# Optimization experiments

Hardware: AMD Instinct MI355X
Metric: run time of the kernel (lower is better)

## Reference

```python
import jax, jax.numpy as jnp
import numpy as np

N_NODES = 50000
N_EDGES = 800000
NUM_GRAPHS = 1024
IN_DIM = 25
DIM = 64
STEPS = 3


def setup_inputs() -> dict:
    key = jax.random.key(0)
    ks = jax.random.split(key, 16)
    s = 0.1
    return {
        "x": jax.random.normal(ks[0], (N_NODES, IN_DIM), dtype=jnp.float32),
        "edge_index": jax.random.randint(ks[1], (2, N_EDGES), 0, N_NODES),
        "batch": jnp.sort(jax.random.randint(ks[2], (N_NODES,), 0, NUM_GRAPHS)),
        "W0": jax.random.normal(ks[3], (IN_DIM, DIM), dtype=jnp.float32) * s,
        "b0": jnp.zeros((DIM,), jnp.float32),
        "Wc": jax.random.normal(ks[4], (DIM, DIM), dtype=jnp.float32) * s,
        "bc": jnp.zeros((DIM,), jnp.float32),
        "Wih": jax.random.normal(ks[5], (4 * DIM, 2 * DIM), dtype=jnp.float32) * s,
        "Whh": jax.random.normal(ks[6], (4 * DIM, DIM), dtype=jnp.float32) * s,
        "bih": jnp.zeros((4 * DIM,), jnp.float32),
        "bhh": jnp.zeros((4 * DIM,), jnp.float32),
        "W1": jax.random.normal(ks[7], (2 * DIM, DIM), dtype=jnp.float32) * s,
        "b1": jnp.zeros((DIM,), jnp.float32),
        "W2": jax.random.normal(ks[8], (DIM, 1), dtype=jnp.float32) * s,
        "b2": jnp.zeros((1,), jnp.float32),
    }


def _lstm_cell(xin, h, c, Wih, Whh, bih, bhh):
    gates = xin @ Wih.T + h @ Whh.T + bih + bhh  # [B, 4*DIM]
    i, f, g, o = jnp.split(gates, 4, axis=-1)
    i, f, o = jax.nn.sigmoid(i), jax.nn.sigmoid(f), jax.nn.sigmoid(o)
    g = jnp.tanh(g)
    c = f * c + i * g
    h = o * jnp.tanh(c)
    return h, c


def reference(x, edge_index, batch, W0, b0, Wc, bc, Wih, Whh, bih, bhh, W1, b1, W2, b2):
    n = x.shape[0]
    # lin0 + relu
    h = jax.nn.relu(x @ W0 + b0)
    # GCNConv: x @ W, add self loops, symmetric normalization, scatter-add
    hw = h @ Wc
    loops = jnp.arange(n, dtype=edge_index.dtype)
    row = jnp.concatenate([edge_index[0], loops])  # sources
    col = jnp.concatenate([edge_index[1], loops])  # targets
    deg = jax.ops.segment_sum(jnp.ones_like(row, dtype=hw.dtype), col, num_segments=n)
    dinv = jnp.where(deg > 0, jax.lax.rsqrt(deg), 0.0)
    norm = dinv[row] * dinv[col]
    msg = hw[row] * norm[:, None]  # [E+N, DIM] gather
    agg = jax.ops.segment_sum(msg, col, num_segments=n) + bc
    h = jax.nn.relu(agg)
    # Set2Set pooling with LSTM, 3 processing steps
    B = NUM_GRAPHS
    q_star = jnp.zeros((B, 2 * DIM), h.dtype)
    hs = jnp.zeros((B, DIM), h.dtype)
    cs = jnp.zeros((B, DIM), h.dtype)
    for _ in range(STEPS):
        hs, cs = _lstm_cell(q_star, hs, cs, Wih, Whh, bih, bhh)
        q = hs  # [B, DIM]
        e = jnp.sum(h * q[batch], axis=-1)  # [N]
        emax = jax.ops.segment_max(e, batch, num_segments=B)
        a = jnp.exp(e - emax[batch])
        asum = jax.ops.segment_sum(a, batch, num_segments=B)
        a = a / asum[batch]
        r = jax.ops.segment_sum(a[:, None] * h, batch, num_segments=B)  # [B, DIM]
        q_star = jnp.concatenate([q, r], axis=-1)
    out = jax.nn.relu(q_star @ W1 + b1)
    out = out @ W2 + b2
    return out.reshape(-1)
```

## Files before the change

### kernel.cpp

```cpp
#include <hip/hip_runtime.h>
#include <hip/hip_fp16.h>
#include <math.h>

#define N_NODES 50000
#define N_EDGES 800000
#define NGRAPH  1024
#define IN_DIM  25
#define DIM     64

#define NBKB 782
#define CAP  1536
#define NBIN 391
#define CROWS 128

__device__ inline float wsum(float v) {
#pragma unroll
  for (int off = 32; off > 0; off >>= 1) v += __shfl_xor(v, off, 64);
  return v;
}
__device__ inline float sigmoidf(float x) { return 1.f / (1.f + expf(-x)); }

__global__ __launch_bounds__(512) void k_bin(const int* __restrict__ ei,
    int* __restrict__ gcur, int* __restrict__ pairs,
    const float* __restrict__ Wih, const float* __restrict__ Whh,
    float* __restrict__ WT) {
  __shared__ int hist[NBKB];
  __shared__ int sbase[NBKB];
  __shared__ int lbase[NBKB];
  __shared__ int sorted[2048];
  int t = threadIdx.x;
  if (blockIdx.x == NBIN) {
    for (int i = t; i < 3 * DIM * 4 * DIM; i += 512) {
      int k = i >> 8, tt = i & 255;
      WT[i] = (k < 2 * DIM) ? Wih[tt * 2 * DIM + k] : Whh[tt * DIM + (k - 2 * DIM)];
    }
    return;
  }
  int base = blockIdx.x * 2048;
  for (int i = t; i < NBKB; i += 512) hist[i] = 0;
  __syncthreads();
  int n = min(2048, N_EDGES - base);
  const int4* r4 = (const int4*)(ei + base);
  const int4* c4 = (const int4*)(ei + N_EDGES + base);
  int pk[4], bkt[4], rank[4];
  {
    bool ok = t * 4 < n;
    int4 rv, cv;
    if (ok) { rv = r4[t]; cv = c4[t]; }
#pragma unroll
    for (int u = 0; u < 4; u++) {
      if (ok) {
        int row = (&rv.x)[u], col = (&cv.x)[u];
        int b = col >> 6;
        bkt[u] = b;
        rank[u] = atomicAdd(&hist[b], 1);
        pk[u] = (int)(((unsigned)b << 22) | ((unsigned)(col & 63) << 16) | (unsigned)row);
      } else {
        bkt[u] = -1;
      }
    }
  }
  __syncthreads();
  if (t < 64) {
    int v[13];
    int loc = 0;
#pragma unroll
    for (int i = 0; i < 13; i++) {
      int idx = t * 13 + i;
      v[i] = (idx < NBKB) ? hist[idx] : 0;
      loc += v[i];
    }
    int x = loc;
#pragma unroll
    for (int d = 1; d < 64; d <<= 1) {
      int y = __shfl_up(x, d, 64);
      if (t >= d) x += y;
    }
    int excl = x - loc;
#pragma unroll
    for (int i = 0; i < 13; i++) {
      int idx = t * 13 + i;
      if (idx < NBKB) sbase[idx] = excl;
      excl += v[i];
    }
  }
  __syncthreads();
#pragma unroll
  for (int u = 0; u < 4; u++)
    if (bkt[u] >= 0) sorted[sbase[bkt[u]] + rank[u]] = pk[u];
  for (int i = t; i < NBKB; i += 512)
    lbase[i] = hist[i] ? atomicAdd(&gcur[i], hist[i]) : 0;
  __syncthreads();
  for (int i = t; i < n; i += 512) {
    int p = sorted[i];
    int b = ((unsigned)p) >> 22;
    int gpos = lbase[b] + (i - sbase[b]);
    if (gpos < CAP) pairs[(size_t)b * CAP + gpos] = p & 0x3FFFFF;
  }
}

__global__ __launch_bounds__(256) void k_lin0(const float* __restrict__ x,
    const float* __restrict__ W0, const float* __restrict__ b0,
    const float* __restrict__ Wc, const int* __restrict__ pairs,
    const int* __restrict__ gcur, float* __restrict__ dinv,
    __half* __restrict__ hw16) {
  __shared__ float sx[64][IN_DIM + 1];
  __shared__ float sW0[IN_DIM][DIM];
  __shared__ float sh[64][DIM + 4];
  __shared__ float sWc[DIM][DIM];
  __shared__ int histd[64];
  int t = threadIdx.x;
  int row0 = blockIdx.x * 64;
  if (t < 64) histd[t] = 0;
  __syncthreads();
  for (int i = t; i < 64 * IN_DIM; i += 256) {
    int r = i / IN_DIM, k = i - r * IN_DIM;
    int row = row0 + r;
    sx[r][k] = (row < N_NODES) ? x[row * IN_DIM + k] : 0.f;
  }
  for (int i = t; i < IN_DIM * DIM; i += 256) sW0[i >> 6][i & 63] = W0[i];
  for (int i = t; i < DIM * DIM; i += 256) sWc[i >> 6][i & 63] = Wc[i];
  {
    int ne = min(gcur[blockIdx.x], CAP);
    const int* pp = pairs + (size_t)blockIdx.x * CAP;
    const int4* pp4 = (const int4*)pp;
    int ne4 = ne >> 2;
    for (int i = t; i < ne4; i += 256) {
      int4 p4 = pp4[i];
      atomicAdd(&histd[(p4.x >> 16) & 63], 1);
      atomicAdd(&histd[(p4.y >> 16) & 63], 1);
      atomicAdd(&histd[(p4.z >> 16) & 63], 1);
      atomicAdd(&histd[(p4.w >> 16) & 63], 1);
    }
    for (int i = (ne4 << 2) + t; i < ne; i += 256)
      atomicAdd(&histd[(pp[i] >> 16) & 63], 1);
  }
  __syncthreads();
  int tc = (t & 15) * 4;
  int tr = (t >> 4) * 4;
  float acc[4][4];
  {
    float4 bb = *(const float4*)&b0[tc];
#pragma unroll
    for (int i = 0; i < 4; i++) {
      acc[i][0] = bb.x; acc[i][1] = bb.y; acc[i][2] = bb.z; acc[i][3] = bb.w;
    }
  }
#pragma unroll
  for (int k = 0; k < IN_DIM; k++) {
    float4 w = *(const float4*)&sW0[k][tc];
#pragma unroll
    for (int i = 0; i < 4; i++) {
      float a = sx[tr + i][k];
      acc[i][0] += a * w.x; acc[i][1] += a * w.y;
      acc[i][2] += a * w.z; acc[i][3] += a * w.w;
    }
  }
#pragma unroll
  for (int i = 0; i < 4; i++) {
    sh[tr + i][tc + 0] = fmaxf(acc[i][0], 0.f);
    sh[tr + i][tc + 1] = fmaxf(acc[i][1], 0.f);
    sh[tr + i][tc + 2] = fmaxf(acc[i][2], 0.f);
    sh[tr + i][tc + 3] = fmaxf(acc[i][3], 0.f);
  }
  __syncthreads();
#pragma unroll
  for (int i = 0; i < 4; i++) acc[i][0] = acc[i][1] = acc[i][2] = acc[i][3] = 0.f;
#pragma unroll 8
  for (int k = 0; k < DIM; k++) {
    float4 w = *(const float4*)&sWc[k][tc];
#pragma unroll
    for (int i = 0; i < 4; i++) {
      float a = sh[tr + i][k];
      acc[i][0] += a * w.x; acc[i][1] += a * w.y;
      acc[i][2] += a * w.z; acc[i][3] += a * w.w;
    }
  }
  if (t < 64) {
    int node = row0 + t;
    if (node < N_NODES) dinv[node] = rsqrtf((float)(histd[t] + 1));
  }
  float2* hwf2 = (float2*)hw16;
#pragma unroll
  for (int i = 0; i < 4; i++) {
    int row = row0 + tr + i;
    if (row < N_NODES) {
      float dv = rsqrtf((float)(histd[tr + i] + 1));
      float2 st;
      ((__half2*)&st)[0] = __floats2half2_rn(acc[i][0] * dv, acc[i][1] * dv);
      ((__half2*)&st)[1] = __floats2half2_rn(acc[i][2] * dv, acc[i][3] * dv);
      hwf2[(size_t)row * 16 + (t & 15)] = st;
    }
  }
}

__global__ __launch_bounds__(256) void k_agg(const int* __restrict__ pairs,
    const int* __restrict__ gcur, const __half* __restrict__ hw16,
    const float* __restrict__ dinv, const float4* __restrict__ bc4,
    __half* __restrict__ h16) {
  __shared__ unsigned short rows[CAP];
  __shared__ int hist[64];
  __shared__ int off[65];
  __shared__ int cur[64];
  int b = blockIdx.x, t = threadIdx.x;
  int lane = t & 63, wave = t >> 6, q = lane >> 4, ql = lane & 15;
  int qid = (wave << 2) + q;
  if (t < 64) hist[t] = 0;
  __syncthreads();
  int ne = min(gcur[b], CAP);
  const int* pp = pairs + (size_t)b * CAP;
  const int4* pp4 = (const int4*)pp;
  int ne4 = ne >> 2;
  for (int i = t; i < ne4; i += 256) {
    int4 p4 = pp4[i];
    atomicAdd(&hist[(p4.x >> 16) & 63], 1);
    atomicAdd(&hist[(p4.y >> 16) & 63], 1);
    atomicAdd(&hist[(p4.z >> 16) & 63], 1);
    atomicAdd(&hist[(p4.w >> 16) & 63], 1);
  }
  for (int i = (ne4 << 2) + t; i < ne; i += 256)
    atomicAdd(&hist[(pp[i] >> 16) & 63], 1);
  __syncthreads();
  if (t < 64) {
    int v = hist[t];
    int x = v;
#pragma unroll
    for (int d = 1; d < 64; d <<= 1) {
      int y = __shfl_up(x, d, 64);
      if (t >= d) x += y;
    }
    off[t] = x - v;
    cur[t] = x - v;
    if (t == 63) off[64] = x;
  }
  __syncthreads();
  for (int i = t; i < ne4; i += 256) {
    int4 p4 = pp4[i];
#pragma unroll
    for (int u = 0; u < 4; u++) {
      int p = (&p4.x)[u];
      int slot = atomicAdd(&cur[(p >> 16) & 63], 1);
      rows[slot] = (unsigned short)(p & 0xFFFF);
    }
  }
  for (int i = (ne4 << 2) + t; i < ne; i += 256) {
    int p = pp[i];
    int slot = atomicAdd(&cur[(p >> 16) & 63], 1);
    rows[slot] = (unsigned short)(p & 0xFFFF);
  }
  __syncthreads();
  const float2* hwf2 = (const float2*)hw16;
  float4 bb = bc4[ql];
  for (int nl = qid; nl < 64; nl += 16) {
    int node = b * 64 + nl;
    if (node >= N_NODES) continue;
    int s0 = off[nl], e0 = off[nl + 1];
    float4 a0, a1, a2, a3;
    {
      float2 raw = hwf2[(size_t)node * 16 + ql];
      float2 f0 = __half22float2(((const __half2*)&raw)[0]);
      float2 f1 = __half22float2(((const __half2*)&raw)[1]);
      a0 = make_float4(f0.x, f0.y, f1.x, f1.y);
      a1 = make_float4(0.f, 0.f, 0.f, 0.f); a2 = a1; a3 = a1;
    }
    int j = s0;
    for (; j + 4 <= e0; j += 4) {
      int r0 = rows[j], r1 = rows[j + 1], r2 = rows[j + 2], r3 = rows[j + 3];
      float2 w0 = hwf2[(size_t)r0 * 16 + ql];
      float2 w1 = hwf2[(size_t)r1 * 16 + ql];
      float2 w2 = hwf2[(size_t)r2 * 16 + ql];
      float2 w3 = hwf2[(size_t)r3 * 16 + ql];
      float2 f;
      f = __half22float2(((const __half2*)&w0)[0]); a0.x += f.x; a0.y += f.y;
      f = __half22float2(((const __half2*)&w0)[1]); a0.z += f.x; a0.w += f.y;
      f = __half22float2(((const __half2*)&w1)[0]); a1.x += f.x; a1.y += f.y;
      f = __half22float2(((const __half2*)&w1)[1]); a1.z += f.x; a1.w += f.y;
      f = __half22float2(((const __half2*)&w2)[0]); a2.x += f.x; a2.y += f.y;
      f = __half22float2(((const __half2*)&w2)[1]); a2.z += f.x; a2.w += f.y;
      f = __half22float2(((const __half2*)&w3)[0]); a3.x += f.x; a3.y += f.y;
      f = __half22float2(((const __half2*)&w3)[1]); a3.z += f.x; a3.w += f.y;
    }
    for (; j < e0; j++) {
      int r = rows[j];
      float2 w = hwf2[(size_t)r * 16 + ql];
      float2 f;
      f = __half22float2(((const __half2*)&w)[0]); a0.x += f.x; a0.y += f.y;
      f = __half22float2(((const __half2*)&w)[1]); a0.z += f.x; a0.w += f.y;
    }
    float di = dinv[node];
    float ox = fmaxf(((a0.x + a1.x) + (a2.x + a3.x)) * di + bb.x, 0.f);
    float oy = fmaxf(((a0.y + a1.y) + (a2.y + a3.y)) * di + bb.y, 0.f);
    float oz = fmaxf(((a0.z + a1.z) + (a2.z + a3.z)) * di + bb.z, 0.f);
    float ow = fmaxf(((a0.w + a1.w) + (a2.w + a3.w)) * di + bb.w, 0.f);
    float2 st;
    ((__half2*)&st)[0] = __floats2half2_rn(ox, oy);
    ((__half2*)&st)[1] = __floats2half2_rn(oz, ow);
    ((float2*)h16)[(size_t)node * 16 + ql] = st;
  }
}

__global__ __launch_bounds__(256) void k_set2set(
    const __half* __restrict__ h16, const int* __restrict__ batch,
    const float* __restrict__ WT, const float* __restrict__ bih,
    const float* __restrict__ bhh, const float* __restrict__ W1,
    const float* __restrict__ b1, const float* __restrict__ W2,
    const float* __restrict__ b2, float* __restrict__ out) {
  int b = blockIdx.x, t = threadIdx.x;
  int wave = t >> 6, lane = t & 63;
  int q = lane >> 4, ql = lane & 15;
  int qid = (wave << 2) + q;
  __shared__ float2 hcf2[CROWS * 16];
  __shared__ float qs[2 * DIM];
  __shared__ float hsl[DIM], csl[DIM];
  __shared__ float gates[4 * DIM];
  __shared__ float red[16 * DIM];
  __shared__ float lred[16], wmax[16];
  __shared__ int seg[2];
  const float2* h2 = (const float2*)h16;
  if (t < 2) {
    int g = b + t;
    int lo = 0, hi = N_NODES;
    if (g == NGRAPH) lo = N_NODES;
    else while (lo < hi) { int mid = (lo + hi) >> 1; if (batch[mid] < g) lo = mid + 1; else hi = mid; }
    seg[t] = lo;
  }
  if (t < 2 * DIM) qs[t] = 0.f;
  if (t < DIM) { hsl[t] = 0.f; csl[t] = 0.f; }
  __syncthreads();
  int s = seg[0], eend = seg[1];
  int nc = min(eend - s, CROWS);
  for (int i = t; i < nc * 16; i += 256)
    hcf2[i] = h2[(size_t)(s + (i >> 4)) * 16 + (i & 15)];
  __syncthreads();
  float bsum = bih[t] + bhh[t];
  for (int step = 0; step < 3; step++) {
    float g = bsum;
    if (step > 0) {
      const float* wp = WT + t;
      float g1 = 0.f;
#pragma unroll 8
      for (int k = 0; k < 2 * DIM; k += 2) {
        g += qs[k] * wp[k * 4 * DIM];
        g1 += qs[k + 1] * wp[(k + 1) * 4 * DIM];
      }
#pragma unroll 8
      for (int k = 0; k < DIM; k += 2) {
        g += hsl[k] * wp[(2 * DIM + k) * 4 * DIM];
        g1 += hsl[k + 1] * wp[(2 * DIM + k + 1) * 4 * DIM];
      }
      g += g1;
    }
    gates[t] = g;
    __syncthreads();
    if (t < DIM) {
      float ig = sigmoidf(gates[t]);
      float fg = sigmoidf(gates[DIM + t]);
      float gg = tanhf(gates[2 * DIM + t]);
      float og = sigmoidf(gates[3 * DIM + t]);
      float c = fg * csl[t] + ig * gg;
      csl[t] = c;
      float hh = og * tanhf(c);
      hsl[t] = hh;
      qs[t] = hh;
    }
    __syncthreads();
    float4 qf = *(const float4*)&hsl[4 * ql];
    float m_w = -INFINITY, l_w = 0.f;
    float4 racc = make_float4(0.f, 0.f, 0.f, 0.f);
    for (int j = s + qid; j < eend; j += 16) {
      int lj = j - s;
      float2 raw = (lj < CROWS) ? hcf2[lj * 16 + ql]
                                : h2[(size_t)j * 16 + ql];
      float2 f0 = __half22float2(((const __half2*)&raw)[0]);
      float2 f1 = __half22float2(((const __half2*)&raw)[1]);
      float p = f0.x * qf.x + f0.y * qf.y + f1.x * qf.z + f1.y * qf.w;
#pragma unroll
      for (int off = 1; off < 16; off <<= 1) p += __shfl_xor(p, off, 64);
      float m_new = fmaxf(m_w, p);
      float scale = __expf(m_w - m_new);
      float a = __expf(p - m_new);
      racc.x = racc.x * scale + a * f0.x;
      racc.y = racc.y * scale + a * f0.y;
      racc.z = racc.z * scale + a * f1.x;
      racc.w = racc.w * scale + a * f1.y;
      l_w = l_w * scale + a;
      m_w = m_new;
    }
    *(float4*)&red[qid * DIM + 4 * ql] = racc;
    if (ql == 0) { lred[qid] = l_w; wmax[qid] = m_w; }
    __syncthreads();
    if (t < DIM) {
      float m_b = -1e30f;
      for (int i = 0; i < 16; i++) m_b = fmaxf(m_b, wmax[i]);
      float r = 0.f, l = 0.f;
      for (int i = 0; i < 16; i++) {
        float e = __expf(wmax[i] - m_b);
        r += red[i * DIM + t] * e;
        l += lred[i] * e;
      }
      qs[DIM + t] = (l > 0.f) ? r / l : 0.f;
    }
    __syncthreads();
  }
  if (t < DIM) {
    float acc = b1[t];
#pragma unroll
    for (int k = 0; k < 2 * DIM; k++) acc += qs[k] * W1[k * DIM + t];
    acc = fmaxf(acc, 0.f);
    float v = wsum(acc * W2[t]);
    if (t == 0) out[b] = v + b2[0];
  }
}

extern "C" void kernel_launch(void* const* d_in, const int* in_sizes, int n_in,
                              void* d_out, int out_size, void* d_ws, size_t ws_size,
                              hipStream_t stream) {
  const float* x    = (const float*)d_in[0];
  const int*   ei   = (const int*)d_in[1];
  const int*   batch= (const int*)d_in[2];
  const float* W0   = (const float*)d_in[3];
  const float* b0   = (const float*)d_in[4];
  const float* Wc   = (const float*)d_in[5];
  const float* bc   = (const float*)d_in[6];
  const float* Wih  = (const float*)d_in[7];
  const float* Whh  = (const float*)d_in[8];
  const float* bih  = (const float*)d_in[9];
  const float* bhh  = (const float*)d_in[10];
  const float* W1   = (const float*)d_in[11];
  const float* b1   = (const float*)d_in[12];
  const float* W2   = (const float*)d_in[13];
  const float* b2   = (const float*)d_in[14];
  float* out = (float*)d_out;

  __half* hw16 = (__half*)d_ws;
  __half* h16  = hw16 + (size_t)N_NODES * DIM;
  float* dinv  = (float*)(h16 + (size_t)N_NODES * DIM);
  float* WT    = dinv + N_NODES;
  int* gcur    = (int*)(WT + 3 * DIM * 4 * DIM);
  int* pairs   = gcur + NBKB + 2;

  hipMemsetAsync(gcur, 0, NBKB * sizeof(int), stream);
  k_bin<<<NBIN + 1, 512, 0, stream>>>(ei, gcur, pairs, Wih, Whh, WT);
  k_lin0<<<NBKB, 256, 0, stream>>>(x, W0, b0, Wc, pairs, gcur, dinv, hw16);
  k_agg<<<NBKB, 256, 0, stream>>>(pairs, gcur, hw16, dinv, (const float4*)bc, h16);
  k_set2set<<<NGRAPH, 256, 0, stream>>>(h16, batch, WT, bih, bhh, W1, b1, W2, b2, out);
}
```

Measured before the change: 191.9 us.

## Batch four graphs per set2set block, enlarge binning blocks, unroll gather by eight

The set2set kernel now handles four graphs per block. Each LSTM weight load is reused across four gate accumulators, and each graph's attention pass is split across four quarter-wave groups, cutting redundant weight traffic and the block count. The binning kernel processes 4096 edges per 1024-thread block, which halves the number of blocks and global atomics. The aggregation gather loop gets an eight-way unrolled path for more loads in flight. The trade-offs are less parallelism per graph in the attention loop and only 256 set2set blocks to fill the device.

```diff
diff --git a/kernel.cpp b/kernel.cpp
--- a/kernel.cpp
+++ b/kernel.cpp
@@ -10,8 +10,10 @@
 
 #define NBKB 782
 #define CAP  1536
-#define NBIN 391
-#define CROWS 128
+#define EPB  4096
+#define NBIN 196
+#define GPB  4
+#define CROW1 64
 
 __device__ inline float wsum(float v) {
 #pragma unroll
@@ -20,26 +22,26 @@
 }
 __device__ inline float sigmoidf(float x) { return 1.f / (1.f + expf(-x)); }
 
-__global__ __launch_bounds__(512) void k_bin(const int* __restrict__ ei,
+__global__ __launch_bounds__(1024) void k_bin(const int* __restrict__ ei,
     int* __restrict__ gcur, int* __restrict__ pairs,
     const float* __restrict__ Wih, const float* __restrict__ Whh,
     float* __restrict__ WT) {
   __shared__ int hist[NBKB];
   __shared__ int sbase[NBKB];
   __shared__ int lbase[NBKB];
-  __shared__ int sorted[2048];
+  __shared__ int sorted[EPB];
   int t = threadIdx.x;
   if (blockIdx.x == NBIN) {
-    for (int i = t; i < 3 * DIM * 4 * DIM; i += 512) {
+    for (int i = t; i < 3 * DIM * 4 * DIM; i += 1024) {
       int k = i >> 8, tt = i & 255;
       WT[i] = (k < 2 * DIM) ? Wih[tt * 2 * DIM + k] : Whh[tt * DIM + (k - 2 * DIM)];
     }
     return;
   }
-  int base = blockIdx.x * 2048;
-  for (int i = t; i < NBKB; i += 512) hist[i] = 0;
-  __syncthreads();
-  int n = min(2048, N_EDGES - base);
+  int base = blockIdx.x * EPB;
+  for (int i = t; i < NBKB; i += 1024) hist[i] = 0;
+  __syncthreads();
+  int n = min(EPB, N_EDGES - base);
   const int4* r4 = (const int4*)(ei + base);
   const int4* c4 = (const int4*)(ei + N_EDGES + base);
   int pk[4], bkt[4], rank[4];
@@ -88,10 +90,10 @@
 #pragma unroll
   for (int u = 0; u < 4; u++)
     if (bkt[u] >= 0) sorted[sbase[bkt[u]] + rank[u]] = pk[u];
-  for (int i = t; i < NBKB; i += 512)
+  for (int i = t; i < NBKB; i += 1024)
     lbase[i] = hist[i] ? atomicAdd(&gcur[i], hist[i]) : 0;
   __syncthreads();
-  for (int i = t; i < n; i += 512) {
+  for (int i = t; i < n; i += 1024) {
     int p = sorted[i];
     int b = ((unsigned)p) >> 22;
     int gpos = lbase[b] + (i - sbase[b]);
@@ -264,6 +266,35 @@
       a1 = make_float4(0.f, 0.f, 0.f, 0.f); a2 = a1; a3 = a1;
     }
     int j = s0;
+    for (; j + 8 <= e0; j += 8) {
+      int r0 = rows[j], r1 = rows[j + 1], r2 = rows[j + 2], r3 = rows[j + 3];
+      int r4_ = rows[j + 4], r5 = rows[j + 5], r6 = rows[j + 6], r7 = rows[j + 7];
+      float2 w0 = hwf2[(size_t)r0 * 16 + ql];
+      float2 w1 = hwf2[(size_t)r1 * 16 + ql];
+      float2 w2 = hwf2[(size_t)r2 * 16 + ql];
+      float2 w3 = hwf2[(size_t)r3 * 16 + ql];
+      float2 w4 = hwf2[(size_t)r4_ * 16 + ql];
+      float2 w5 = hwf2[(size_t)r5 * 16 + ql];
+      float2 w6 = hwf2[(size_t)r6 * 16 + ql];
+      float2 w7 = hwf2[(size_t)r7 * 16 + ql];
+      float2 f;
+      f = __half22float2(((const __half2*)&w0)[0]); a0.x += f.x; a0.y += f.y;
+      f = __half22float2(((const __half2*)&w0)[1]); a0.z += f.x; a0.w += f.y;
+      f = __half22float2(((const __half2*)&w1)[0]); a1.x += f.x; a1.y += f.y;
+      f = __half22float2(((const __half2*)&w1)[1]); a1.z += f.x; a1.w += f.y;
+      f = __half22float2(((const __half2*)&w2)[0]); a2.x += f.x; a2.y += f.y;
+      f = __half22float2(((const __half2*)&w2)[1]); a2.z += f.x; a2.w += f.y;
+      f = __half22float2(((const __half2*)&w3)[0]); a3.x += f.x; a3.y += f.y;
+      f = __half22float2(((const __half2*)&w3)[1]); a3.z += f.x; a3.w += f.y;
+      f = __half22float2(((const __half2*)&w4)[0]); a0.x += f.x; a0.y += f.y;
+      f = __half22float2(((const __half2*)&w4)[1]); a0.z += f.x; a0.w += f.y;
+      f = __half22float2(((const __half2*)&w5)[0]); a1.x += f.x; a1.y += f.y;
+      f = __half22float2(((const __half2*)&w5)[1]); a1.z += f.x; a1.w += f.y;
+      f = __half22float2(((const __half2*)&w6)[0]); a2.x += f.x; a2.y += f.y;
+      f = __half22float2(((const __half2*)&w6)[1]); a2.z += f.x; a2.w += f.y;
+      f = __half22float2(((const __half2*)&w7)[0]); a3.x += f.x; a3.y += f.y;
+      f = __half22float2(((const __half2*)&w7)[1]); a3.z += f.x; a3.w += f.y;
+    }
     for (; j + 4 <= e0; j += 4) {
       int r0 = rows[j], r1 = rows[j + 1], r2 = rows[j + 2], r3 = rows[j + 3];
       float2 w0 = hwf2[(size_t)r0 * 16 + ql];
@@ -309,67 +340,81 @@
   int wave = t >> 6, lane = t & 63;
   int q = lane >> 4, ql = lane & 15;
   int qid = (wave << 2) + q;
-  __shared__ float2 hcf2[CROWS * 16];
-  __shared__ float qs[2 * DIM];
-  __shared__ float hsl[DIM], csl[DIM];
-  __shared__ float gates[4 * DIM];
+  __shared__ float2 hcf2[GPB * CROW1 * 16];
+  __shared__ float qs4[GPB * 2 * DIM];
+  __shared__ float hsl4[GPB * DIM], csl4[GPB * DIM];
+  __shared__ float gates4[GPB * 4 * DIM];
   __shared__ float red[16 * DIM];
   __shared__ float lred[16], wmax[16];
-  __shared__ int seg[2];
+  __shared__ int seg[GPB + 1];
   const float2* h2 = (const float2*)h16;
-  if (t < 2) {
-    int g = b + t;
+  if (t < GPB + 1) {
+    int g = b * GPB + t;
     int lo = 0, hi = N_NODES;
-    if (g == NGRAPH) lo = N_NODES;
+    if (g >= NGRAPH) lo = N_NODES;
     else while (lo < hi) { int mid = (lo + hi) >> 1; if (batch[mid] < g) lo = mid + 1; else hi = mid; }
     seg[t] = lo;
   }
-  if (t < 2 * DIM) qs[t] = 0.f;
-  if (t < DIM) { hsl[t] = 0.f; csl[t] = 0.f; }
-  __syncthreads();
-  int s = seg[0], eend = seg[1];
-  int nc = min(eend - s, CROWS);
-  for (int i = t; i < nc * 16; i += 256)
-    hcf2[i] = h2[(size_t)(s + (i >> 4)) * 16 + (i & 15)];
+  for (int i = t; i < GPB * 2 * DIM; i += 256) qs4[i] = 0.f;
+  if (t < GPB * DIM) { hsl4[t] = 0.f; csl4[t] = 0.f; }
+  __syncthreads();
+  for (int i = t; i < GPB * CROW1 * 16; i += 256) {
+    int g = i >> 10;
+    int lj = (i >> 4) & (CROW1 - 1);
+    int row = seg[g] + lj;
+    if (row < seg[g + 1]) hcf2[i] = h2[(size_t)row * 16 + (i & 15)];
+  }
   __syncthreads();
   float bsum = bih[t] + bhh[t];
+  int ga = qid & 3;
+  int sub = qid >> 2;
   for (int step = 0; step < 3; step++) {
-    float g = bsum;
+    float g0 = bsum, g1 = bsum, g2 = bsum, g3 = bsum;
     if (step > 0) {
       const float* wp = WT + t;
-      float g1 = 0.f;
-#pragma unroll 8
-      for (int k = 0; k < 2 * DIM; k += 2) {
-        g += qs[k] * wp[k * 4 * DIM];
-        g1 += qs[k + 1] * wp[(k + 1) * 4 * DIM];
+#pragma unroll 4
+      for (int k = 0; k < 2 * DIM; k++) {
+        float w = wp[k * 4 * DIM];
+        g0 += qs4[0 * 2 * DIM + k] * w;
+        g1 += qs4[1 * 2 * DIM + k] * w;
+        g2 += qs4[2 * 2 * DIM + k] * w;
+        g3 += qs4[3 * 2 * DIM + k] * w;
       }
-#pragma unroll 8
-      for (int k = 0; k < DIM; k += 2) {
-        g += hsl[k] * wp[(2 * DIM + k) * 4 * DIM];
-        g1 += hsl[k + 1] * wp[(2 * DIM + k + 1) * 4 * DIM];
+#pragma unroll 4
+      for (int k = 0; k < DIM; k++) {
+        float w = wp[(2 * DIM + k) * 4 * DIM];
+        g0 += hsl4[0 * DIM + k] * w;
+        g1 += hsl4[1 * DIM + k] * w;
+        g2 += hsl4[2 * DIM + k] * w;
+        g3 += hsl4[3 * DIM + k] * w;
       }
-      g += g1;
-    }
-    gates[t] = g;
+    }
+    gates4[0 * 4 * DIM + t] = g0;
+    gates4[1 * 4 * DIM + t] = g1;
+    gates4[2 * 4 * DIM + t] = g2;
+    gates4[3 * 4 * DIM + t] = g3;
     __syncthreads();
-    if (t < DIM) {
-      float ig = sigmoidf(gates[t]);
-      float fg = sigmoidf(gates[DIM + t]);
-      float gg = tanhf(gates[2 * DIM + t]);
-      float og = sigmoidf(gates[3 * DIM + t]);
-      float c = fg * csl[t] + ig * gg;
-      csl[t] = c;
+    {
+      int g = wave, j = lane;
+      const float* gg_ = &gates4[g * 4 * DIM];
+      float ig = sigmoidf(gg_[j]);
+      float fg = sigmoidf(gg_[DIM + j]);
+      float gv = tanhf(gg_[2 * DIM + j]);
+      float og = sigmoidf(gg_[3 * DIM + j]);
+      float c = fg * csl4[g * DIM + j] + ig * gv;
+      csl4[g * DIM + j] = c;
       float hh = og * tanhf(c);
-      hsl[t] = hh;
-      qs[t] = hh;
+      hsl4[g * DIM + j] = hh;
+      qs4[g * 2 * DIM + j] = hh;
     }
     __syncthreads();
-    float4 qf = *(const float4*)&hsl[4 * ql];
+    float4 qf = *(const float4*)&hsl4[ga * DIM + 4 * ql];
     float m_w = -INFINITY, l_w = 0.f;
     float4 racc = make_float4(0.f, 0.f, 0.f, 0.f);
-    for (int j = s + qid; j < eend; j += 16) {
-      int lj = j - s;
-      float2 raw = (lj < CROWS) ? hcf2[lj * 16 + ql]
+    int s_g = seg[ga], e_g = seg[ga + 1];
+    for (int j = s_g + sub; j < e_g; j += 4) {
+      int lj = j - s_g;
+      float2 raw = (lj < CROW1) ? hcf2[(ga * CROW1 + lj) * 16 + ql]
                                 : h2[(size_t)j * 16 + ql];
       float2 f0 = __half22float2(((const __half2*)&raw)[0]);
       float2 f1 = __half22float2(((const __half2*)&raw)[1]);
@@ -389,26 +434,31 @@
     *(float4*)&red[qid * DIM + 4 * ql] = racc;
     if (ql == 0) { lred[qid] = l_w; wmax[qid] = m_w; }
     __syncthreads();
-    if (t < DIM) {
+    {
+      int g = wave, j = lane;
       float m_b = -1e30f;
-      for (int i = 0; i < 16; i++) m_b = fmaxf(m_b, wmax[i]);
+#pragma unroll
+      for (int i = 0; i < 4; i++) m_b = fmaxf(m_b, wmax[g + 4 * i]);
       float r = 0.f, l = 0.f;
-      for (int i = 0; i < 16; i++) {
-        float e = __expf(wmax[i] - m_b);
-        r += red[i * DIM + t] * e;
-        l += lred[i] * e;
+#pragma unroll
+      for (int i = 0; i < 4; i++) {
+        int qi = g + 4 * i;
+        float e = __expf(wmax[qi] - m_b);
+        r += red[qi * DIM + j] * e;
+        l += lred[qi] * e;
       }
-      qs[DIM + t] = (l > 0.f) ? r / l : 0.f;
+      qs4[g * 2 * DIM + DIM + j] = (l > 0.f) ? r / l : 0.f;
     }
     __syncthreads();
   }
-  if (t < DIM) {
-    float acc = b1[t];
-#pragma unroll
-    for (int k = 0; k < 2 * DIM; k++) acc += qs[k] * W1[k * DIM + t];
+  {
+    int g = wave, j = lane;
+    float acc = b1[j];
+#pragma unroll 4
+    for (int k = 0; k < 2 * DIM; k++) acc += qs4[g * 2 * DIM + k] * W1[k * DIM + j];
     acc = fmaxf(acc, 0.f);
-    float v = wsum(acc * W2[t]);
-    if (t == 0) out[b] = v + b2[0];
+    float v = wsum(acc * W2[j]);
+    if (j == 0) out[b * GPB + g] = v + b2[0];
   }
 }
 
@@ -440,8 +490,8 @@
   int* pairs   = gcur + NBKB + 2;
 
   hipMemsetAsync(gcur, 0, NBKB * sizeof(int), stream);
-  k_bin<<<NBIN + 1, 512, 0, stream>>>(ei, gcur, pairs, Wih, Whh, WT);
+  k_bin<<<NBIN + 1, 1024, 0, stream>>>(ei, gcur, pairs, Wih, Whh, WT);
   k_lin0<<<NBKB, 256, 0, stream>>>(x, W0, b0, Wc, pairs, gcur, dinv, hw16);
   k_agg<<<NBKB, 256, 0, stream>>>(pairs, gcur, hw16, dinv, (const float4*)bc, h16);
-  k_set2set<<<NGRAPH, 256, 0, stream>>>(h16, batch, WT, bih, bhh, W1, b1, W2, b2, out);
-}
+  k_set2set<<<NGRAPH / GPB, 256, 0, stream>>>(h16, batch, WT, bih, bhh, W1, b1, W2, b2, out);
+}
```

New measurement: 210.9 us. 9.9% more time.
